# Performance work log

Hardware: AMD Instinct MI355X
Metric: run time of the kernel (lower is better)

The kernel has to match this reference:

```python
import jax, jax.numpy as jnp
import numpy as np

EPS = 1e-9

def _cheb_attention_conv(X_real, X_imag, lap_real, lap_imag,
                         Wa_real, Wa_imag, ba_real, ba_imag,
                         modrelu_b, W_real, W_imag):
    B, N, C = X_real.shape
    # --- attention scores: CVLinear over cat([x_i, x_j]) == (X@W1)_i + (X@W2)_j + b ---
    W1r, W2r = Wa_real[:C, 0], Wa_real[C:, 0]  # [C]
    W1i, W2i = Wa_imag[:C, 0], Wa_imag[C:, 0]
    # complex matvec: (Xr + iXi)(Wr + iWi)
    si_r = X_real @ W1r - X_imag @ W1i          # [B,N] contribution of x_i
    si_i = X_real @ W1i + X_imag @ W1r
    sj_r = X_real @ W2r - X_imag @ W2i          # [B,N] contribution of x_j
    sj_i = X_real @ W2i + X_imag @ W2r
    sc_r = si_r[:, :, None] + sj_r[:, None, :] + ba_real[0]   # [B,N,N]
    sc_i = si_i[:, :, None] + sj_i[:, None, :] + ba_imag[0]
    # --- learnable modReLU: relu(|z| + b) * z/|z| ---
    mag = jnp.sqrt(sc_r * sc_r + sc_i * sc_i)
    scale = jax.nn.relu(mag + modrelu_b[0]) / (mag + EPS)
    sc_r = sc_r * scale
    sc_i = sc_i * scale
    # --- split complex softmax over last dim ---
    a_r = jax.nn.softmax(sc_r, axis=-1)
    a_i = jax.nn.softmax(sc_i, axis=-1)
    # --- reweight Laplacian polynomials (complex mult, broadcast over k) ---
    L_r = lap_real * a_r[:, None] - lap_imag * a_i[:, None]   # [B,K+1,N,N]
    L_i = lap_real * a_i[:, None] + lap_imag * a_r[:, None]
    # --- sum_k (L_k X) W_k, complex ---
    LX_r = jnp.einsum('bkij,bjc->bkic', L_r, X_real) - jnp.einsum('bkij,bjc->bkic', L_i, X_imag)
    LX_i = jnp.einsum('bkij,bjc->bkic', L_r, X_imag) + jnp.einsum('bkij,bjc->bkic', L_i, X_real)
    out_r = jnp.einsum('bkic,kco->bio', LX_r, W_real) - jnp.einsum('bkic,kco->bio', LX_i, W_imag)
    out_i = jnp.einsum('bkic,kco->bio', LX_r, W_imag) + jnp.einsum('bkic,kco->bio', LX_i, W_real)
    return out_r, out_i


def setup_inputs() -> dict:
    key = jax.random.key(0)
    ks = jax.random.split(key, 8)
    B, N, C, CO, K1 = 48, 512, 64, 64, 5
    # weights normalized to unit complex magnitude like the torch init
    wr = jax.random.uniform(ks[4], (K1, C, CO), minval=-1.0, maxval=1.0) / np.sqrt(CO)
    wi = jax.random.uniform(ks[5], (K1, C, CO), minval=-1.0, maxval=1.0) / np.sqrt(CO)
    m = jnp.sqrt(wr * wr + wi * wi)
    return {
        'X_real': jax.random.normal(ks[0], (B, N, C), jnp.float32),
        'X_imag': jax.random.normal(ks[1], (B, N, C), jnp.float32),
        'lap_real': jax.random.normal(ks[2], (B, K1, N, N), jnp.float32) * 0.1,
        'lap_imag': jax.random.normal(ks[3], (B, K1, N, N), jnp.float32) * 0.1,
        'Wa_real': jax.random.normal(ks[6], (2 * C, 1), jnp.float32) * 0.1,
        'Wa_imag': jax.random.normal(ks[7], (2 * C, 1), jnp.float32) * 0.1,
        'ba_real': jnp.zeros((1,), jnp.float32),
        'ba_imag': jnp.zeros((1,), jnp.float32),
        'modrelu_b': jnp.zeros((1,), jnp.float32),
        'W_real': (wr / m).astype(jnp.float32),
        'W_imag': (wi / m).astype(jnp.float32),
    }


def reference(X_real, X_imag, lap_real, lap_imag, Wa_real, Wa_imag,
              ba_real, ba_imag, modrelu_b, W_real, W_imag):
    out_r, out_i = _cheb_attention_conv(X_real, X_imag, lap_real, lap_imag,
                                        Wa_real, Wa_imag, ba_real, ba_imag,
                                        modrelu_b, W_real, W_imag)
    return out_r, out_i
```

## Files before the change

### kernel.cpp

```cpp
#include <hip/hip_runtime.h>

#define EPSF 1e-9f

typedef __attribute__((ext_vector_type(8))) short short8;
typedef __attribute__((ext_vector_type(4))) float f32x4;
typedef __attribute__((ext_vector_type(4))) unsigned int u32x4;
typedef __attribute__((ext_vector_type(2))) unsigned int u32x2;

__device__ __forceinline__ unsigned pkbf(float lo, float hi) {
  unsigned r;
  asm("v_cvt_pk_bf16_f32 %0, %1, %2" : "=v"(r) : "v"(lo), "v"(hi));
  return r;
}
__device__ __forceinline__ short8 mk8(unsigned a, unsigned b, unsigned c, unsigned d) {
  u32x4 u = {a, b, c, d};
  return __builtin_bit_cast(short8, u);
}

__global__ __launch_bounds__(256) void k_s(
    const float* __restrict__ Xr, const float* __restrict__ Xi,
    const float* __restrict__ War, const float* __restrict__ Wai,
    float4* __restrict__ s4, float2* __restrict__ sj2)
{
  int t = threadIdx.x;
  int nf = blockIdx.x * 32 + (t >> 3);
  int c0 = (t & 7) * 8;
  const f32x4* xr = (const f32x4*)(Xr + (size_t)nf * 64 + c0);
  const f32x4* xi = (const f32x4*)(Xi + (size_t)nf * 64 + c0);
  const f32x4* w1r = (const f32x4*)(War + c0);
  const f32x4* w2r = (const f32x4*)(War + 64 + c0);
  const f32x4* w1i = (const f32x4*)(Wai + c0);
  const f32x4* w2i = (const f32x4*)(Wai + 64 + c0);
  float sir = 0.f, sii = 0.f, sjr = 0.f, sji = 0.f;
#pragma unroll
  for (int h = 0; h < 2; ++h) {
    f32x4 a = xr[h], bb = xi[h];
    f32x4 u1r = w1r[h], u1i = w1i[h], u2r = w2r[h], u2i = w2i[h];
#pragma unroll
    for (int e = 0; e < 4; ++e) {
      sir += a[e] * u1r[e] - bb[e] * u1i[e];
      sii += a[e] * u1i[e] + bb[e] * u1r[e];
      sjr += a[e] * u2r[e] - bb[e] * u2i[e];
      sji += a[e] * u2i[e] + bb[e] * u2r[e];
    }
  }
#pragma unroll
  for (int off = 1; off < 8; off <<= 1) {
    sir += __shfl_xor(sir, off);
    sii += __shfl_xor(sii, off);
    sjr += __shfl_xor(sjr, off);
    sji += __shfl_xor(sji, off);
  }
  if ((t & 7) == 0) {
    s4[nf] = make_float4(sir, sii, sjr, sji);
    sj2[nf] = make_float2(sjr, sji);
  }
}

__global__ __launch_bounds__(256) void k_stats(
    const float4* __restrict__ s4, const float2* __restrict__ sj2,
    const float* __restrict__ bar, const float* __restrict__ bai,
    const float* __restrict__ modbp, float4* __restrict__ stats)
{
  __shared__ float2 sh[512];
  int t = threadIdx.x;
  int b = blockIdx.x >> 4;
  int i0 = (blockIdx.x & 15) * 32;
  sh[t] = sj2[(size_t)b * 512 + t];
  sh[t + 256] = sj2[(size_t)b * 512 + t + 256];
  __syncthreads();
  float ba_r = bar[0], ba_i = bai[0], modb = modbp[0];
  int i = i0 + (t >> 3), jl = t & 7;
  float4 sv = s4[(size_t)b * 512 + i];
  float sirb = sv.x + ba_r, siib = sv.y + ba_i;
  float mr = -1e30f, mi = -1e30f;
  for (int jj = 0; jj < 64; ++jj) {
    float2 sj = sh[jl * 64 + jj];
    float scr = sirb + sj.x, sci = siib + sj.y;
    float mag = sqrtf(scr * scr + sci * sci);
    float sc = fmaxf(mag + modb, 0.f) * __builtin_amdgcn_rcpf(mag + EPSF);
    mr = fmaxf(mr, scr * sc);
    mi = fmaxf(mi, sci * sc);
  }
#pragma unroll
  for (int off = 1; off < 8; off <<= 1) {
    mr = fmaxf(mr, __shfl_xor(mr, off));
    mi = fmaxf(mi, __shfl_xor(mi, off));
  }
  float er = 0.f, ei = 0.f;
  for (int jj = 0; jj < 64; ++jj) {
    float2 sj = sh[jl * 64 + jj];
    float scr = sirb + sj.x, sci = siib + sj.y;
    float mag = sqrtf(scr * scr + sci * sci);
    float sc = fmaxf(mag + modb, 0.f) * __builtin_amdgcn_rcpf(mag + EPSF);
    er += __expf(scr * sc - mr);
    ei += __expf(sci * sc - mi);
  }
#pragma unroll
  for (int off = 1; off < 8; off <<= 1) {
    er += __shfl_xor(er, off);
    ei += __shfl_xor(ei, off);
  }
  if (jl == 0)
    stats[(size_t)b * 512 + i] = make_float4(mr, 1.f / er, mi, 1.f / ei);
}

__global__ __launch_bounds__(256) void k_y(
    const float* __restrict__ Xr, const float* __restrict__ Xi,
    const float* __restrict__ Wr, const float* __restrict__ Wi,
    u32x4* __restrict__ yfrag)
{
  __shared__ __align__(16) short WtR[64 * 72];
  __shared__ __align__(16) short WtI[64 * 72];
  __shared__ __align__(16) short Yt[4][2][64 * 24];
  int bk = blockIdx.x;
  int b = bk / 5, k = bk % 5;
  int t = threadIdx.x;
  {
    int o = t & 63, cbase = (t >> 6) * 16;
    const float* wr = Wr + (size_t)k * 4096;
    const float* wi = Wi + (size_t)k * 4096;
#pragma unroll
    for (int cc = 0; cc < 16; cc += 2) {
      int c = cbase + cc;
      *(unsigned*)&WtR[o * 72 + c] = pkbf(wr[c * 64 + o], wr[(c + 1) * 64 + o]);
      *(unsigned*)&WtI[o * 72 + c] = pkbf(wi[c * 64 + o], wi[(c + 1) * 64 + o]);
    }
  }
  __syncthreads();
  int w = t >> 6, l = t & 63;
  int lane15 = l & 15, quad = l >> 4;
  short* ytR = &Yt[w][0][0];
  short* ytI = &Yt[w][1][0];
  for (int qq = 0; qq < 8; ++qq) {
    int q = w * 8 + qq;
    int j = q * 16 + lane15;
    const f32x4* pxr = (const f32x4*)(Xr + ((size_t)b * 512 + j) * 64 + quad * 8);
    const f32x4* pxi = (const f32x4*)(Xi + ((size_t)b * 512 + j) * 64 + quad * 8);
    f32x4 xr0 = pxr[0], xr1 = pxr[1], xr8 = pxr[8], xr9 = pxr[9];
    f32x4 xi0 = pxi[0], xi1 = pxi[1], xi8 = pxi[8], xi9 = pxi[9];
    short8 axr[2], axi[2];
    axr[0] = mk8(pkbf(xr0[0], xr0[1]), pkbf(xr0[2], xr0[3]), pkbf(xr1[0], xr1[1]), pkbf(xr1[2], xr1[3]));
    axr[1] = mk8(pkbf(xr8[0], xr8[1]), pkbf(xr8[2], xr8[3]), pkbf(xr9[0], xr9[1]), pkbf(xr9[2], xr9[3]));
    axi[0] = mk8(pkbf(xi0[0], xi0[1]), pkbf(xi0[2], xi0[3]), pkbf(xi1[0], xi1[1]), pkbf(xi1[2], xi1[3]));
    axi[1] = mk8(pkbf(xi8[0], xi8[1]), pkbf(xi8[2], xi8[3]), pkbf(xi9[0], xi9[1]), pkbf(xi9[2], xi9[3]));
    f32x4 aR1[4], aR2[4], aI[4];
#pragma unroll
    for (int os = 0; os < 4; ++os) {
      aR1[os] = f32x4{0.f, 0.f, 0.f, 0.f};
      aR2[os] = f32x4{0.f, 0.f, 0.f, 0.f};
      aI[os] = f32x4{0.f, 0.f, 0.f, 0.f};
    }
#pragma unroll
    for (int kc = 0; kc < 2; ++kc) {
#pragma unroll
      for (int os = 0; os < 4; ++os) {
        int widx = (os * 16 + lane15) * 72 + kc * 32 + quad * 8;
        short8 wrF = *(const short8*)&WtR[widx];
        short8 wiF = *(const short8*)&WtI[widx];
        aR1[os] = __builtin_amdgcn_mfma_f32_16x16x32_bf16(axr[kc], wrF, aR1[os], 0, 0, 0);
        aR2[os] = __builtin_amdgcn_mfma_f32_16x16x32_bf16(axi[kc], wiF, aR2[os], 0, 0, 0);
        aI[os]  = __builtin_amdgcn_mfma_f32_16x16x32_bf16(axr[kc], wiF, aI[os], 0, 0, 0);
        aI[os]  = __builtin_amdgcn_mfma_f32_16x16x32_bf16(axi[kc], wrF, aI[os], 0, 0, 0);
      }
    }
#pragma unroll
    for (int os = 0; os < 4; ++os) {
      f32x4 R = aR1[os] - aR2[os];
      f32x4 I = aI[os];
      int ya = (os * 16 + lane15) * 24 + quad * 4;
      *(u32x2*)&ytR[ya] = u32x2{pkbf(R[0], R[1]), pkbf(R[2], R[3])};
      *(u32x2*)&ytI[ya] = u32x2{pkbf(I[0], I[1]), pkbf(I[2], I[3])};
    }
#pragma unroll
    for (int part = 0; part < 2; ++part) {
      const short* yt = part ? ytI : ytR;
#pragma unroll
      for (int h = 0; h < 2; ++h) {
        short8 unit = *(const short8*)&yt[l * 24 + h * 8];
        size_t line = (((size_t)(b * 5 + k) * 2 + part) * 16 + (q >> 1)) * 4 + (l >> 4);
        size_t idx = line * 64 + ((q & 1) * 2 + h) * 16 + (l & 15);
        yfrag[idx] = __builtin_bit_cast(u32x4, unit);
      }
    }
  }
}

__global__ __launch_bounds__(256, 4) void k_main(
    const float* __restrict__ lapr, const float* __restrict__ lapi,
    const float4* __restrict__ s4, const float4* __restrict__ stats,
    const float2* __restrict__ sj2, const u32x4* __restrict__ yfrag,
    const float* __restrict__ bar, const float* __restrict__ bai,
    const float* __restrict__ modbp,
    float* __restrict__ out_r, float* __restrict__ out_i)
{
  __shared__ __align__(16) f32x4 red[2][64][8];

  const int g = blockIdx.x;
  const int b = (g & 7) + ((g >> 8) << 3);
  const int it = (g >> 3) & 31;
  const int t = threadIdx.x;
  const int w = t >> 6;
  const int l = t & 63;
  const int lane15 = l & 15, quad = l >> 4;
  const int gi = it * 16 + lane15;

  float ba_r = bar[0], ba_i = bai[0], modb = modbp[0];
  float4 sv = s4[(size_t)b * 512 + gi];
  float4 st = stats[(size_t)b * 512 + gi];
  float sirb = sv.x + ba_r, siib = sv.y + ba_i;
  float maxr = st.x, rsr = st.y, maxi = st.z, rsi = st.w;

  f32x4 accR[4], accI[4];
#pragma unroll
  for (int os = 0; os < 4; ++os) {
    accR[os] = f32x4{0.f, 0.f, 0.f, 0.f};
    accI[os] = f32x4{0.f, 0.f, 0.f, 0.f};
  }

  const size_t NN = (size_t)512 * 512;
  const float* lapr_b = lapr + ((size_t)b * 5 * 512 + gi) * 512;
  const float* lapi_b = lapi + ((size_t)b * 5 * 512 + gi) * 512;
  const u32x4* yb = yfrag + (size_t)b * 5 * 8192 + l;

  for (int jsw = 0; jsw < 4; ++jsw) {
    const int js = w * 4 + jsw;
    const int jq = js * 32 + quad * 8;

    const f32x4* sjp = (const f32x4*)(sj2 + (size_t)b * 512 + jq);
    f32x4 sjv0 = sjp[0], sjv1 = sjp[1], sjv2 = sjp[2], sjv3 = sjp[3];
    float sjr[8] = {sjv0[0], sjv0[2], sjv1[0], sjv1[2], sjv2[0], sjv2[2], sjv3[0], sjv3[2]};
    float sjimag[8] = {sjv0[1], sjv0[3], sjv1[1], sjv1[3], sjv2[1], sjv2[3], sjv3[1], sjv3[3]};

    float ar[8], ai[8];
#pragma unroll
    for (int e = 0; e < 8; ++e) {
      float scr = sirb + sjr[e];
      float sci = siib + sjimag[e];
      float mag = __builtin_amdgcn_sqrtf(fmaf(scr, scr, sci * sci));
      float sc = fmaxf(mag + modb, 0.f) * __builtin_amdgcn_rcpf(mag + EPSF);
      ar[e] = __expf(fmaf(scr, sc, -maxr)) * rsr;
      ai[e] = __expf(fmaf(sci, sc, -maxi)) * rsi;
    }

    unsigned pAr[5][4], pAi[5][4];
#pragma unroll
    for (int k = 0; k < 5; ++k) {
      const f32x4* pr = (const f32x4*)(lapr_b + (size_t)k * NN + jq);
      const f32x4* pi_ = (const f32x4*)(lapi_b + (size_t)k * NN + jq);
      f32x4 LR0 = __builtin_nontemporal_load(pr);
      f32x4 LR1 = __builtin_nontemporal_load(pr + 1);
      f32x4 LI0 = __builtin_nontemporal_load(pi_);
      f32x4 LI1 = __builtin_nontemporal_load(pi_ + 1);
      float lrv[8], liv[8];
#pragma unroll
      for (int e = 0; e < 4; ++e) {
        lrv[e]     = LR0[e] * ar[e]     - LI0[e] * ai[e];
        liv[e]     = LR0[e] * ai[e]     + LI0[e] * ar[e];
        lrv[4 + e] = LR1[e] * ar[4 + e] - LI1[e] * ai[4 + e];
        liv[4 + e] = LR1[e] * ai[4 + e] + LI1[e] * ar[4 + e];
      }
      pAr[k][0] = pkbf(lrv[0], lrv[1]); pAr[k][1] = pkbf(lrv[2], lrv[3]);
      pAr[k][2] = pkbf(lrv[4], lrv[5]); pAr[k][3] = pkbf(lrv[6], lrv[7]);
      pAi[k][0] = pkbf(liv[0], liv[1]); pAi[k][1] = pkbf(liv[2], liv[3]);
      pAi[k][2] = pkbf(liv[4], liv[5]); pAi[k][3] = pkbf(liv[6], liv[7]);
    }

#pragma unroll
    for (int k = 0; k < 5; ++k) {
      const u32x4* yk = yb + (size_t)k * 8192 + (size_t)(js * 4) * 64;
      short8 Ar = mk8(pAr[k][0], pAr[k][1], pAr[k][2], pAr[k][3]);
      short8 Ai = mk8(pAi[k][0], pAi[k][1], pAi[k][2], pAi[k][3]);
      short8 An = mk8(pAi[k][0] ^ 0x80008000u, pAi[k][1] ^ 0x80008000u,
                      pAi[k][2] ^ 0x80008000u, pAi[k][3] ^ 0x80008000u);
#pragma unroll
      for (int os = 0; os < 4; ++os) {
        short8 br8 = __builtin_bit_cast(short8, yk[os * 64]);
        short8 bi8 = __builtin_bit_cast(short8, yk[4096 + os * 64]);
        accR[os] = __builtin_amdgcn_mfma_f32_16x16x32_bf16(Ar, br8, accR[os], 0, 0, 0);
        accR[os] = __builtin_amdgcn_mfma_f32_16x16x32_bf16(An, bi8, accR[os], 0, 0, 0);
        accI[os] = __builtin_amdgcn_mfma_f32_16x16x32_bf16(Ar, bi8, accI[os], 0, 0, 0);
        accI[os] = __builtin_amdgcn_mfma_f32_16x16x32_bf16(Ai, br8, accI[os], 0, 0, 0);
      }
    }
  }

  if (w >= 2) {
#pragma unroll
    for (int os = 0; os < 4; ++os) {
      red[w - 2][l][os] = accR[os];
      red[w - 2][l][4 + os] = accI[os];
    }
  }
  __syncthreads();
  if (w < 2) {
#pragma unroll
    for (int os = 0; os < 4; ++os) {
      accR[os] += red[w][l][os];
      accI[os] += red[w][l][4 + os];
    }
  }
  __syncthreads();
  if (w == 1) {
#pragma unroll
    for (int os = 0; os < 4; ++os) {
      red[0][l][os] = accR[os];
      red[0][l][4 + os] = accI[os];
    }
  }
  __syncthreads();
  if (w == 0) {
#pragma unroll
    for (int os = 0; os < 4; ++os) {
      accR[os] += red[0][l][os];
      accI[os] += red[0][l][4 + os];
      int oc = os * 16 + lane15;
#pragma unroll
      for (int r = 0; r < 4; ++r) {
        size_t oidx = ((size_t)b * 512 + it * 16 + quad * 4 + r) * 64 + oc;
        out_r[oidx] = accR[os][r];
        out_i[oidx] = accI[os][r];
      }
    }
  }
}

extern "C" void kernel_launch(void* const* d_in, const int* in_sizes, int n_in,
                              void* d_out, int out_size, void* d_ws, size_t ws_size,
                              hipStream_t stream) {
  const float* Xr = (const float*)d_in[0];
  const float* Xi = (const float*)d_in[1];
  const float* lapr = (const float*)d_in[2];
  const float* lapi = (const float*)d_in[3];
  const float* War = (const float*)d_in[4];
  const float* Wai = (const float*)d_in[5];
  const float* bar = (const float*)d_in[6];
  const float* bai = (const float*)d_in[7];
  const float* modb = (const float*)d_in[8];
  const float* Wr = (const float*)d_in[9];
  const float* Wi = (const float*)d_in[10];

  char* wsb = (char*)d_ws;
  float4* s4 = (float4*)wsb;
  float4* stats = (float4*)(wsb + 393216);
  float2* sj2 = (float2*)(wsb + 786432);
  u32x4* yfrag = (u32x4*)(wsb + 983040);

  float* out_r = (float*)d_out;
  float* out_i = out_r + (size_t)48 * 512 * 64;

  k_s<<<768, 256, 0, stream>>>(Xr, Xi, War, Wai, s4, sj2);
  k_stats<<<768, 256, 0, stream>>>(s4, sj2, bar, bai, modb, stats);
  k_y<<<240, 256, 0, stream>>>(Xr, Xi, Wr, Wi, yfrag);
  k_main<<<1536, 256, 0, stream>>>(lapr, lapi, s4, stats, sj2, yfrag,
                                   bar, bai, modb, out_r, out_i);
}
```

Measured before the change: 212.4 us.

## Precompute attention weights in separate kernel and split main kernel by Chebyshev order

The softmaxed attention coefficients are computed once per (b,i,j) in a new kernel and stored as bf16 fragments, so the main kernel no longer recomputes sqrt/exp for every block. The main kernel now uses 5 waves, each handling one Chebyshev order k over all j, followed by an LDS reduction across waves. k_y is also split into four times as many blocks for more parallelism. This adds extra global traffic for the attention fragments (about 50 MB written and read) and rounds the attention weights to bf16 before they multiply the Laplacian.

```diff
diff --git a/kernel.cpp b/kernel.cpp
--- a/kernel.cpp
+++ b/kernel.cpp
@@ -105,6 +105,50 @@
     stats[(size_t)b * 512 + i] = make_float4(mr, 1.f / er, mi, 1.f / ei);
 }
 
+__global__ __launch_bounds__(256) void k_a(
+    const float4* __restrict__ s4, const float4* __restrict__ stats,
+    const float2* __restrict__ sj2,
+    const float* __restrict__ bar, const float* __restrict__ bai,
+    const float* __restrict__ modbp,
+    u32x4* __restrict__ afrag)
+{
+  int g = blockIdx.x;
+  int b = g >> 5, it = g & 31;
+  int t = threadIdx.x;
+  int l = t & 63, row = l & 15, quad = l >> 4;
+  int wjs = t >> 6;
+  float ba_r = bar[0], ba_i = bai[0], modb = modbp[0];
+  int gi = it * 16 + row;
+  float4 sv = s4[(size_t)b * 512 + gi];
+  float4 st = stats[(size_t)b * 512 + gi];
+  float sirb = sv.x + ba_r, siib = sv.y + ba_i;
+  float maxr = st.x, rsr = st.y, maxi = st.z, rsi = st.w;
+
+  for (int q4 = 0; q4 < 4; ++q4) {
+    int js = q4 * 4 + wjs;
+    int jq = js * 32 + quad * 8;
+    const f32x4* sjp = (const f32x4*)(sj2 + (size_t)b * 512 + jq);
+    f32x4 s0 = sjp[0], s1 = sjp[1], s2 = sjp[2], s3 = sjp[3];
+    float sjr[8] = {s0[0], s0[2], s1[0], s1[2], s2[0], s2[2], s3[0], s3[2]};
+    float sji[8] = {s0[1], s0[3], s1[1], s1[3], s2[1], s2[3], s3[1], s3[3]};
+    float ar[8], ai[8];
+#pragma unroll
+    for (int e = 0; e < 8; ++e) {
+      float scr = sirb + sjr[e];
+      float sci = siib + sji[e];
+      float mag = __builtin_amdgcn_sqrtf(fmaf(scr, scr, sci * sci));
+      float sc = fmaxf(mag + modb, 0.f) * __builtin_amdgcn_rcpf(mag + EPSF);
+      ar[e] = __expf(fmaf(scr, sc, -maxr)) * rsr;
+      ai[e] = __expf(fmaf(sci, sc, -maxi)) * rsi;
+    }
+    u32x4 par = {pkbf(ar[0], ar[1]), pkbf(ar[2], ar[3]), pkbf(ar[4], ar[5]), pkbf(ar[6], ar[7])};
+    u32x4 pai = {pkbf(ai[0], ai[1]), pkbf(ai[2], ai[3]), pkbf(ai[4], ai[5]), pkbf(ai[6], ai[7])};
+    size_t base = ((size_t)g * 16 + js) * 128 + l;
+    afrag[base] = par;
+    afrag[base + 64] = pai;
+  }
+}
+
 __global__ __launch_bounds__(256) void k_y(
     const float* __restrict__ Xr, const float* __restrict__ Xi,
     const float* __restrict__ Wr, const float* __restrict__ Wi,
@@ -113,7 +157,8 @@
   __shared__ __align__(16) short WtR[64 * 72];
   __shared__ __align__(16) short WtI[64 * 72];
   __shared__ __align__(16) short Yt[4][2][64 * 24];
-  int bk = blockIdx.x;
+  int bk = blockIdx.x >> 2;
+  int jh = blockIdx.x & 3;
   int b = bk / 5, k = bk % 5;
   int t = threadIdx.x;
   {
@@ -132,8 +177,8 @@
   int lane15 = l & 15, quad = l >> 4;
   short* ytR = &Yt[w][0][0];
   short* ytI = &Yt[w][1][0];
-  for (int qq = 0; qq < 8; ++qq) {
-    int q = w * 8 + qq;
+  for (int qq = 0; qq < 2; ++qq) {
+    int q = jh * 8 + w * 2 + qq;
     int j = q * 16 + lane15;
     const f32x4* pxr = (const f32x4*)(Xr + ((size_t)b * 512 + j) * 64 + quad * 8);
     const f32x4* pxi = (const f32x4*)(Xi + ((size_t)b * 512 + j) * 64 + quad * 8);
@@ -186,31 +231,23 @@
   }
 }
 
-__global__ __launch_bounds__(256, 4) void k_main(
+__global__ __launch_bounds__(320, 4) void k_main(
     const float* __restrict__ lapr, const float* __restrict__ lapi,
-    const float4* __restrict__ s4, const float4* __restrict__ stats,
-    const float2* __restrict__ sj2, const u32x4* __restrict__ yfrag,
-    const float* __restrict__ bar, const float* __restrict__ bai,
-    const float* __restrict__ modbp,
+    const u32x4* __restrict__ afrag, const u32x4* __restrict__ yfrag,
     float* __restrict__ out_r, float* __restrict__ out_i)
 {
-  __shared__ __align__(16) f32x4 red[2][64][8];
+  __shared__ float red[4][2][4][4][64];
 
   const int g = blockIdx.x;
   const int b = (g & 7) + ((g >> 8) << 3);
   const int it = (g >> 3) & 31;
+  const int g2 = b * 32 + it;
   const int t = threadIdx.x;
   const int w = t >> 6;
   const int l = t & 63;
   const int lane15 = l & 15, quad = l >> 4;
   const int gi = it * 16 + lane15;
 
-  float ba_r = bar[0], ba_i = bai[0], modb = modbp[0];
-  float4 sv = s4[(size_t)b * 512 + gi];
-  float4 st = stats[(size_t)b * 512 + gi];
-  float sirb = sv.x + ba_r, siib = sv.y + ba_i;
-  float maxr = st.x, rsr = st.y, maxi = st.z, rsi = st.w;
-
   f32x4 accR[4], accI[4];
 #pragma unroll
   for (int os = 0; os < 4; ++os) {
@@ -218,102 +255,82 @@
     accI[os] = f32x4{0.f, 0.f, 0.f, 0.f};
   }
 
-  const size_t NN = (size_t)512 * 512;
-  const float* lapr_b = lapr + ((size_t)b * 5 * 512 + gi) * 512;
-  const float* lapi_b = lapi + ((size_t)b * 5 * 512 + gi) * 512;
-  const u32x4* yb = yfrag + (size_t)b * 5 * 8192 + l;
-
-  for (int jsw = 0; jsw < 4; ++jsw) {
-    const int js = w * 4 + jsw;
+  const float* lapr_w = lapr + ((size_t)(b * 5 + w) * 512 + gi) * 512;
+  const float* lapi_w = lapi + ((size_t)(b * 5 + w) * 512 + gi) * 512;
+  const u32x4* yw = yfrag + (size_t)(b * 5 + w) * 8192 + l;
+  const u32x4* aw = afrag + (size_t)g2 * 2048 + l;
+
+  for (int js = 0; js < 16; ++js) {
     const int jq = js * 32 + quad * 8;
-
-    const f32x4* sjp = (const f32x4*)(sj2 + (size_t)b * 512 + jq);
-    f32x4 sjv0 = sjp[0], sjv1 = sjp[1], sjv2 = sjp[2], sjv3 = sjp[3];
-    float sjr[8] = {sjv0[0], sjv0[2], sjv1[0], sjv1[2], sjv2[0], sjv2[2], sjv3[0], sjv3[2]};
-    float sjimag[8] = {sjv0[1], sjv0[3], sjv1[1], sjv1[3], sjv2[1], sjv2[3], sjv3[1], sjv3[3]};
+    const f32x4* pr = (const f32x4*)(lapr_w + jq);
+    const f32x4* pi_ = (const f32x4*)(lapi_w + jq);
+    f32x4 LR0 = __builtin_nontemporal_load(pr);
+    f32x4 LR1 = __builtin_nontemporal_load(pr + 1);
+    f32x4 LI0 = __builtin_nontemporal_load(pi_);
+    f32x4 LI1 = __builtin_nontemporal_load(pi_ + 1);
+    u32x4 par = aw[js * 128];
+    u32x4 pai = aw[js * 128 + 64];
 
     float ar[8], ai[8];
 #pragma unroll
-    for (int e = 0; e < 8; ++e) {
-      float scr = sirb + sjr[e];
-      float sci = siib + sjimag[e];
-      float mag = __builtin_amdgcn_sqrtf(fmaf(scr, scr, sci * sci));
-      float sc = fmaxf(mag + modb, 0.f) * __builtin_amdgcn_rcpf(mag + EPSF);
-      ar[e] = __expf(fmaf(scr, sc, -maxr)) * rsr;
-      ai[e] = __expf(fmaf(sci, sc, -maxi)) * rsi;
-    }
-
-    unsigned pAr[5][4], pAi[5][4];
-#pragma unroll
-    for (int k = 0; k < 5; ++k) {
-      const f32x4* pr = (const f32x4*)(lapr_b + (size_t)k * NN + jq);
-      const f32x4* pi_ = (const f32x4*)(lapi_b + (size_t)k * NN + jq);
-      f32x4 LR0 = __builtin_nontemporal_load(pr);
-      f32x4 LR1 = __builtin_nontemporal_load(pr + 1);
-      f32x4 LI0 = __builtin_nontemporal_load(pi_);
-      f32x4 LI1 = __builtin_nontemporal_load(pi_ + 1);
-      float lrv[8], liv[8];
-#pragma unroll
-      for (int e = 0; e < 4; ++e) {
-        lrv[e]     = LR0[e] * ar[e]     - LI0[e] * ai[e];
-        liv[e]     = LR0[e] * ai[e]     + LI0[e] * ar[e];
-        lrv[4 + e] = LR1[e] * ar[4 + e] - LI1[e] * ai[4 + e];
-        liv[4 + e] = LR1[e] * ai[4 + e] + LI1[e] * ar[4 + e];
+    for (int d = 0; d < 4; ++d) {
+      ar[2 * d]     = __builtin_bit_cast(float, par[d] << 16);
+      ar[2 * d + 1] = __builtin_bit_cast(float, par[d] & 0xffff0000u);
+      ai[2 * d]     = __builtin_bit_cast(float, pai[d] << 16);
+      ai[2 * d + 1] = __builtin_bit_cast(float, pai[d] & 0xffff0000u);
+    }
+
+    float lrv[8], liv[8];
+#pragma unroll
+    for (int e = 0; e < 4; ++e) {
+      lrv[e]     = LR0[e] * ar[e]     - LI0[e] * ai[e];
+      liv[e]     = LR0[e] * ai[e]     + LI0[e] * ar[e];
+      lrv[4 + e] = LR1[e] * ar[4 + e] - LI1[e] * ai[4 + e];
+      liv[4 + e] = LR1[e] * ai[4 + e] + LI1[e] * ar[4 + e];
+    }
+    unsigned p0 = pkbf(lrv[0], lrv[1]), p1 = pkbf(lrv[2], lrv[3]);
+    unsigned p2 = pkbf(lrv[4], lrv[5]), p3 = pkbf(lrv[6], lrv[7]);
+    unsigned q0 = pkbf(liv[0], liv[1]), q1 = pkbf(liv[2], liv[3]);
+    unsigned q2 = pkbf(liv[4], liv[5]), q3 = pkbf(liv[6], liv[7]);
+    short8 Ar = mk8(p0, p1, p2, p3);
+    short8 Ai = mk8(q0, q1, q2, q3);
+    short8 An = mk8(q0 ^ 0x80008000u, q1 ^ 0x80008000u,
+                    q2 ^ 0x80008000u, q3 ^ 0x80008000u);
+
+    const u32x4* yk = yw + (size_t)(js * 4) * 64;
+#pragma unroll
+    for (int os = 0; os < 4; ++os) {
+      short8 br8 = __builtin_bit_cast(short8, yk[os * 64]);
+      short8 bi8 = __builtin_bit_cast(short8, yk[4096 + os * 64]);
+      accR[os] = __builtin_amdgcn_mfma_f32_16x16x32_bf16(Ar, br8, accR[os], 0, 0, 0);
+      accR[os] = __builtin_amdgcn_mfma_f32_16x16x32_bf16(An, bi8, accR[os], 0, 0, 0);
+      accI[os] = __builtin_amdgcn_mfma_f32_16x16x32_bf16(Ar, bi8, accI[os], 0, 0, 0);
+      accI[os] = __builtin_amdgcn_mfma_f32_16x16x32_bf16(Ai, br8, accI[os], 0, 0, 0);
+    }
+  }
+
+  if (w > 0) {
+#pragma unroll
+    for (int os = 0; os < 4; ++os)
+#pragma unroll
+      for (int c = 0; c < 4; ++c) {
+        red[w - 1][0][os][c][l] = accR[os][c];
+        red[w - 1][1][os][c][l] = accI[os][c];
       }
-      pAr[k][0] = pkbf(lrv[0], lrv[1]); pAr[k][1] = pkbf(lrv[2], lrv[3]);
-      pAr[k][2] = pkbf(lrv[4], lrv[5]); pAr[k][3] = pkbf(lrv[6], lrv[7]);
-      pAi[k][0] = pkbf(liv[0], liv[1]); pAi[k][1] = pkbf(liv[2], liv[3]);
-      pAi[k][2] = pkbf(liv[4], liv[5]); pAi[k][3] = pkbf(liv[6], liv[7]);
-    }
-
-#pragma unroll
-    for (int k = 0; k < 5; ++k) {
-      const u32x4* yk = yb + (size_t)k * 8192 + (size_t)(js * 4) * 64;
-      short8 Ar = mk8(pAr[k][0], pAr[k][1], pAr[k][2], pAr[k][3]);
-      short8 Ai = mk8(pAi[k][0], pAi[k][1], pAi[k][2], pAi[k][3]);
-      short8 An = mk8(pAi[k][0] ^ 0x80008000u, pAi[k][1] ^ 0x80008000u,
-                      pAi[k][2] ^ 0x80008000u, pAi[k][3] ^ 0x80008000u);
-#pragma unroll
-      for (int os = 0; os < 4; ++os) {
-        short8 br8 = __builtin_bit_cast(short8, yk[os * 64]);
-        short8 bi8 = __builtin_bit_cast(short8, yk[4096 + os * 64]);
-        accR[os] = __builtin_amdgcn_mfma_f32_16x16x32_bf16(Ar, br8, accR[os], 0, 0, 0);
-        accR[os] = __builtin_amdgcn_mfma_f32_16x16x32_bf16(An, bi8, accR[os], 0, 0, 0);
-        accI[os] = __builtin_amdgcn_mfma_f32_16x16x32_bf16(Ar, bi8, accI[os], 0, 0, 0);
-        accI[os] = __builtin_amdgcn_mfma_f32_16x16x32_bf16(Ai, br8, accI[os], 0, 0, 0);
-      }
-    }
-  }
-
-  if (w >= 2) {
-#pragma unroll
-    for (int os = 0; os < 4; ++os) {
-      red[w - 2][l][os] = accR[os];
-      red[w - 2][l][4 + os] = accI[os];
-    }
-  }
-  __syncthreads();
-  if (w < 2) {
-#pragma unroll
-    for (int os = 0; os < 4; ++os) {
-      accR[os] += red[w][l][os];
-      accI[os] += red[w][l][4 + os];
-    }
-  }
-  __syncthreads();
-  if (w == 1) {
-#pragma unroll
-    for (int os = 0; os < 4; ++os) {
-      red[0][l][os] = accR[os];
-      red[0][l][4 + os] = accI[os];
-    }
   }
   __syncthreads();
   if (w == 0) {
 #pragma unroll
+    for (int wv = 0; wv < 4; ++wv)
+#pragma unroll
+      for (int os = 0; os < 4; ++os)
+#pragma unroll
+        for (int c = 0; c < 4; ++c) {
+          accR[os][c] += red[wv][0][os][c][l];
+          accI[os][c] += red[wv][1][os][c][l];
+        }
+#pragma unroll
     for (int os = 0; os < 4; ++os) {
-      accR[os] += red[0][l][os];
-      accI[os] += red[0][l][4 + os];
       int oc = os * 16 + lane15;
 #pragma unroll
       for (int r = 0; r < 4; ++r) {
@@ -345,13 +362,14 @@
   float4* stats = (float4*)(wsb + 393216);
   float2* sj2 = (float2*)(wsb + 786432);
   u32x4* yfrag = (u32x4*)(wsb + 983040);
+  u32x4* afrag = (u32x4*)(wsb + 983040 + 31457280);
 
   float* out_r = (float*)d_out;
   float* out_i = out_r + (size_t)48 * 512 * 64;
 
   k_s<<<768, 256, 0, stream>>>(Xr, Xi, War, Wai, s4, sj2);
   k_stats<<<768, 256, 0, stream>>>(s4, sj2, bar, bai, modb, stats);
-  k_y<<<240, 256, 0, stream>>>(Xr, Xi, Wr, Wi, yfrag);
-  k_main<<<1536, 256, 0, stream>>>(lapr, lapi, s4, stats, sj2, yfrag,
-                                   bar, bai, modb, out_r, out_i);
-}
+  k_a<<<1536, 256, 0, stream>>>(s4, stats, sj2, bar, bai, modb, afrag);
+  k_y<<<960, 256, 0, stream>>>(Xr, Xi, Wr, Wi, yfrag);
+  k_main<<<1536, 320, 0, stream>>>(lapr, lapi, afrag, yfrag, out_r, out_i);
+}
```

Result: slower. 233.9 us (+10.1%).
